# Performance work log

Hardware: AMD Instinct MI355X
Metric: run time of the kernel (lower is better)

The kernel has to match this reference:

```python
import jax, jax.numpy as jnp
import numpy as np

B, S, C, H, FF = 2, 1500, 1024, 16, 4096
D = C // H  # head_dim = 64
EPS = 1e-5


def _ln(x, g, b):
    # LayerNorm over channel dim (axis=1) for (B, C, S) tensors
    mu = jnp.mean(x, axis=1, keepdims=True)
    var = jnp.mean(jnp.square(x - mu), axis=1, keepdims=True)
    return (x - mu) * jax.lax.rsqrt(var + EPS) * g[None, :, None] + b[None, :, None]


def setup_inputs() -> dict:
    key = jax.random.key(0)
    ks = jax.random.split(key, 24)
    w = lambda k, shp: (jax.random.normal(k, shp, dtype=jnp.float32) * 0.02)
    return {
        "hidden_states": jax.random.normal(ks[0], (B, C, 1, S), dtype=jnp.float32),
        "attention_mask": jnp.ones((B, S), dtype=jnp.float32),
        "position_bias": jax.random.normal(ks[1], (B, H, S, S), dtype=jnp.float32),
        "Wq": w(ks[2], (C, C)), "bq": jnp.zeros((C,), jnp.float32),
        "Wk": w(ks[3], (C, C)), "bk": jnp.zeros((C,), jnp.float32),
        "Wv": w(ks[4], (C, C)), "bv": jnp.zeros((C,), jnp.float32),
        "Wo": w(ks[5], (C, C)), "bo": jnp.zeros((C,), jnp.float32),
        "Wg": w(ks[6], (8, D)), "bg": jnp.zeros((8,), jnp.float32),
        "gru_const": jnp.ones((1, 1, H, 1), jnp.float32),
        "ln1_g": jnp.ones((C,), jnp.float32), "ln1_b": jnp.zeros((C,), jnp.float32),
        "W1": w(ks[7], (FF, C)), "b1": jnp.zeros((FF,), jnp.float32),
        "W2": w(ks[8], (C, FF)), "b2": jnp.zeros((C,), jnp.float32),
        "ln2_g": jnp.ones((C,), jnp.float32), "ln2_b": jnp.zeros((C,), jnp.float32),
    }


def reference(hidden_states, attention_mask, position_bias,
              Wq, bq, Wk, bk, Wv, bv, Wo, bo, Wg, bg, gru_const,
              ln1_g, ln1_b, W1, b1, W2, b2, ln2_g, ln2_b):
    x = hidden_states[:, :, 0, :]  # (B, C, S)

    # --- GRU-style relative-position gate ---
    xh = x.reshape(B, H, D, S)  # (B, H, D, S)
    # conv2d with (8, D, 1, 1) kernel on (B, D, H, S) == per-head linear D->8
    g8 = jnp.einsum('od,bhds->bohs', Wg, xh) + bg[None, :, None, None]  # (B, 8, H, S)
    gate_a = jax.nn.sigmoid(jnp.sum(g8[:, :4], axis=1, keepdims=True))  # (B, 1, H, S)
    gate_b = jax.nn.sigmoid(jnp.sum(g8[:, 4:], axis=1, keepdims=True))  # (B, 1, H, S)
    gate = gate_a * (gate_b * gru_const - 1.0) + 2.0  # (B, 1, H, S)
    qk_mask = gate[:, 0, :, :, None] * position_bias  # (B, H, Sq, Sk)

    # --- self-attention ---
    q = (jnp.einsum('oc,bcs->bos', Wq, x) + bq[None, :, None]).reshape(B, H, D, S)
    k = (jnp.einsum('oc,bcs->bos', Wk, x) + bk[None, :, None]).reshape(B, H, D, S)
    v = (jnp.einsum('oc,bcs->bos', Wv, x) + bv[None, :, None]).reshape(B, H, D, S)
    scale = 1.0 / jnp.sqrt(jnp.float32(D))
    kpm = (1.0 - attention_mask) * -10000.0  # (B, S)
    scores = jnp.einsum('bhdq,bhdk->bhqk', q, k) * scale + qk_mask + kpm[:, None, None, :]
    probs = jax.nn.softmax(scores, axis=-1)
    ctx = jnp.einsum('bhqk,bhdk->bhdq', probs, v).reshape(B, C, S)
    attn_out = jnp.einsum('oc,bcs->bos', Wo, ctx) + bo[None, :, None]

    h = _ln(x + attn_out, ln1_g, ln1_b)

    # --- FFN ---
    f = jax.nn.gelu(jnp.einsum('fc,bcs->bfs', W1, h) + b1[None, :, None], approximate=False)
    f = jnp.einsum('cf,bfs->bcs', W2, f) + b2[None, :, None]

    out = _ln(h + f, ln2_g, ln2_b)
    return out[:, :, None, :]  # (B, C, 1, S)
```

## Files before the change

kernel.cpp:

```cpp
#include <hip/hip_runtime.h>
#include <cstddef>
#include <cstdint>

#define Bn 2
#define Sn 1500
#define SPn 1536
#define Cn 1024
#define Hn 16
#define FFn 4096

typedef __attribute__((ext_vector_type(8))) short bf16x8;
typedef __attribute__((ext_vector_type(4))) float f32x4;
typedef unsigned short u16;
typedef unsigned int u32;

__device__ __forceinline__ u16 f2bu(float f) {
  unsigned u = __float_as_uint(f);
  return (u16)((u + 0x7fffu + ((u >> 16) & 1u)) >> 16);
}
__device__ __forceinline__ float bu2f(u16 v) {
  return __uint_as_float(((u32)v) << 16);
}

__device__ __forceinline__ void gl_lds16(const u16* g, u16* l) {
  __builtin_amdgcn_global_load_lds(
      (__attribute__((address_space(1))) void*)(uintptr_t)g,
      (__attribute__((address_space(3))) void*)(u32)(uintptr_t)l,
      16, 0, 0);
}

__global__ __launch_bounds__(256) void k_pre(
    const float* __restrict__ x,
    const float* __restrict__ Wq, const float* __restrict__ Wk,
    const float* __restrict__ Wv, const float* __restrict__ Wo,
    const float* __restrict__ W1, const float* __restrict__ W2,
    const float* __restrict__ bq, const float* __restrict__ bk,
    const float* __restrict__ bv,
    const float* __restrict__ Wg, const float* __restrict__ bg,
    const float* __restrict__ gc,
    float* __restrict__ xT, u16* __restrict__ xTb,
    u16* __restrict__ wqkvb, u16* __restrict__ wob,
    u16* __restrict__ w1b, u16* __restrict__ w2b, float* __restrict__ bqkv,
    float* __restrict__ gate)
{
  const int bid = blockIdx.x;
  if (bid < 3072) {
    __shared__ float t[32][33];
    const int c0 = (bid & 31) * 32, s0 = ((bid >> 5) % 48) * 32, b = bid / 1536;
    const int tx = threadIdx.x & 31, ty = threadIdx.x >> 5;
#pragma unroll
    for (int i = 0; i < 32; i += 8) {
      int c = c0 + ty + i, s = s0 + tx;
      t[ty + i][tx] = (s < Sn) ? x[((size_t)b * Cn + c) * Sn + s] : 0.f;
    }
    __syncthreads();
#pragma unroll
    for (int i = 0; i < 32; i += 8) {
      int s = s0 + ty + i, c = c0 + tx;
      float v = t[tx][ty + i];
      size_t o = ((size_t)b * SPn + s) * Cn + c;
      xT[o] = v;
      xTb[o] = f2bu(v);
    }
    return;
  }
  if (bid < 15363) {
    int i = (bid - 3072) * 256 + threadIdx.x;
    const float* src;
    u16* dst;
    int j;
    if (i < 786432) {
      src = (i < 262144) ? Wq : ((i < 524288) ? Wk : Wv);
      j = i & 262143;
      dst = wqkvb + (size_t)i * 4;
    } else if (i < 1048576) {
      src = Wo; j = i - 786432; dst = wob + (size_t)j * 4;
    } else if (i < 2097152) {
      src = W1; j = i - 1048576; dst = w1b + (size_t)j * 4;
    } else if (i < 3145728) {
      src = W2; j = i - 2097152; dst = w2b + (size_t)j * 4;
    } else {
      int k = i - 3145728;
      const float* bsrc = (k < 256) ? bq : ((k < 512) ? bk : bv);
      float4 v = *(const float4*)(bsrc + (k & 255) * 4);
      *(float4*)(bqkv + k * 4) = v;
      return;
    }
    float4 v = *(const float4*)(src + (size_t)j * 4);
    ushort4 o;
    o.x = f2bu(v.x); o.y = f2bu(v.y); o.z = f2bu(v.z); o.w = f2bu(v.w);
    *(ushort4*)dst = o;
    return;
  }
  {
    const int gid = bid - 15363;
    const int b = gid / 96, h = (gid / 6) & 15;
    const int s = (gid % 6) * 256 + threadIdx.x;
    const bool vld = s < Sn;
    const float* xp = x + ((size_t)b * Cn + h * 64) * Sn + (vld ? s : 0);
    float dot[8];
#pragma unroll
    for (int o = 0; o < 8; o++) dot[o] = 0.f;
    for (int d = 0; d < 64; d++) {
      float v = xp[(size_t)d * Sn];
#pragma unroll
      for (int o = 0; o < 8; o++) dot[o] += Wg[o * 64 + d] * v;
    }
    float sa = dot[0] + dot[1] + dot[2] + dot[3] + bg[0] + bg[1] + bg[2] + bg[3];
    float sb = dot[4] + dot[5] + dot[6] + dot[7] + bg[4] + bg[5] + bg[6] + bg[7];
    float ga = 1.f / (1.f + __expf(-sa));
    float gb = 1.f / (1.f + __expf(-sb));
    float gv = ga * (gb * gc[h] - 1.f) + 2.f;
    gate[((size_t)b * Hn + h) * SPn + s] = vld ? gv : 0.f;
  }
}

__global__ __launch_bounds__(256) void k_transpose_out(
    const float* __restrict__ oT, float* __restrict__ o)
{
  __shared__ float t[32][33];
  const int b = blockIdx.z, c0 = blockIdx.x * 32, s0 = blockIdx.y * 32;
  const int tx = threadIdx.x & 31, ty = threadIdx.x >> 5;
#pragma unroll
  for (int i = 0; i < 32; i += 8) {
    int s = s0 + ty + i, c = c0 + tx;
    t[ty + i][tx] = oT[((size_t)b * SPn + s) * Cn + c];
  }
  __syncthreads();
#pragma unroll
  for (int i = 0; i < 32; i += 8) {
    int c = c0 + ty + i, s = s0 + tx;
    if (s < Sn) o[((size_t)b * Cn + c) * Sn + s] = t[tx][ty + i];
  }
}

template <int EPI, int SPLIT, int TM>
__global__ __launch_bounds__(256) void k_gemm(
    const u16* __restrict__ A, const u16* __restrict__ X,
    const float* __restrict__ bias, void* __restrict__ out, void* __restrict__ out2,
    u16* __restrict__ vT, int M, int Kst, int Ktot)
{
  constexpr int NI = TM / 32;
  const int zz = blockIdx.z;
  const int b = zz / SPLIT, half = zz % SPLIT;
  const int Kc = Ktot / SPLIT;
  const int m0 = blockIdx.x * TM;
  const int s0 = blockIdx.y * 128;
  const int tid = threadIdx.x;
  const int lane = tid & 63;
  const int wid = tid >> 6;
  const int wm = (wid >> 1) * (TM / 2);
  const int wn = (wid & 1) * 64;
  const int l15 = lane & 15;
  const int g4 = lane >> 4;

  __shared__ __align__(16) u16 lA[TM][64];
  __shared__ __align__(16) u16 lX[128][64];

  f32x4 acc[NI][4];
  f32x4 zr; zr[0] = 0.f; zr[1] = 0.f; zr[2] = 0.f; zr[3] = 0.f;
#pragma unroll
  for (int i = 0; i < NI; i++)
#pragma unroll
    for (int j = 0; j < 4; j++) acc[i][j] = zr;

  const int rlo = lane >> 3;
  const int cg = (lane & 7) ^ rlo;
  const int kbeg = half * Kc;
  const u16* gA = A + (size_t)(m0 + wid * (TM / 4) + rlo) * Kst + cg * 8 + kbeg;
  const u16* gX = X + ((size_t)b * SPn + s0 + wid * 32 + rlo) * Kst + cg * 8 + kbeg;
  u16* lAp = &lA[0][0] + wid * (TM / 4) * 64;
  u16* lXp = &lX[0][0] + wid * 2048;
  const size_t rstep8 = (size_t)8 * Kst;

  for (int kt = 0; kt < Kc; kt += 64) {
    __syncthreads();
#pragma unroll
    for (int j = 0; j < TM / 32; j++)
      gl_lds16(gA + j * rstep8 + kt, lAp + j * 512);
#pragma unroll
    for (int j = 0; j < 4; j++)
      gl_lds16(gX + j * rstep8 + kt, lXp + j * 512);
    __syncthreads();
#pragma unroll
    for (int ks = 0; ks < 2; ks++) {
      bf16x8 af[NI], bfr[4];
#pragma unroll
      for (int i = 0; i < NI; i++) {
        int ra = wm + i * 16 + l15;
        af[i] = *(const bf16x8*)&lA[ra][((ks * 4 + g4) ^ (ra & 7)) * 8];
      }
#pragma unroll
      for (int j = 0; j < 4; j++) {
        int rb = wn + j * 16 + l15;
        bfr[j] = *(const bf16x8*)&lX[rb][((ks * 4 + g4) ^ (rb & 7)) * 8];
      }
#pragma unroll
      for (int i = 0; i < NI; i++)
#pragma unroll
        for (int j = 0; j < 4; j++)
          acc[i][j] = __builtin_amdgcn_mfma_f32_16x16x32_bf16(af[i], bfr[j], acc[i][j], 0, 0, 0);
    }
  }

  const float hsc = (half == 0) ? 1.f : 0.f;
  void* outp = (half == 0) ? out : out2;
#pragma unroll
  for (int i = 0; i < NI; i++) {
    int o = m0 + wm + i * 16 + g4 * 4;
    float4 bs = *(const float4*)(bias + o);
#pragma unroll
    for (int j = 0; j < 4; j++) {
      int s = s0 + wn + j * 16 + l15;
      size_t oidx = ((size_t)b * SPn + s) * M + o;
      f32x4 v = acc[i][j];
      float x0 = v[0] + bs.x * hsc, x1 = v[1] + bs.y * hsc;
      float x2 = v[2] + bs.z * hsc, x3 = v[3] + bs.w * hsc;
      if (EPI == 0) {
        float4 st; st.x = x0; st.y = x1; st.z = x2; st.w = x3;
        *(float4*)((float*)outp + oidx) = st;
      } else if (EPI == 1) {
        x0 = 0.5f * x0 * (1.f + erff(x0 * 0.70710678118654752f));
        x1 = 0.5f * x1 * (1.f + erff(x1 * 0.70710678118654752f));
        x2 = 0.5f * x2 * (1.f + erff(x2 * 0.70710678118654752f));
        x3 = 0.5f * x3 * (1.f + erff(x3 * 0.70710678118654752f));
        ushort4 st;
        st.x = f2bu(x0); st.y = f2bu(x1); st.z = f2bu(x2); st.w = f2bu(x3);
        *(ushort4*)((u16*)outp + oidx) = st;
      } else {
        ushort4 st;
        st.x = f2bu(x0); st.y = f2bu(x1); st.z = f2bu(x2); st.w = f2bu(x3);
        *(ushort4*)((u16*)outp + oidx) = st;
        if (vT != nullptr && o >= 2048) {
          int oo = o - 2048;
          int h = oo >> 6, d = oo & 63;
          u16* vp = vT + ((size_t)(b * Hn + h) * 64 + d) * SPn + s;
          vp[0] = st.x;
          vp[SPn] = st.y;
          vp[2 * SPn] = st.z;
          vp[3 * SPn] = st.w;
        }
      }
    }
  }
}

__global__ __launch_bounds__(256) void k_flash_mfma(
    const u16* __restrict__ qkv,
    const u16* __restrict__ vT,
    const float* __restrict__ pb,
    const float* __restrict__ am,
    const float* __restrict__ gate,
    u16* __restrict__ ctx)
{
  const int bh = blockIdx.y, b = bh >> 4, h = bh & 15;
  const int q0 = blockIdx.x * 64;
  const int tid = threadIdx.x;
  const int lane = tid & 63, wid = tid >> 6;
  const int l15 = lane & 15, g4 = lane >> 4;
  const int q = q0 + wid * 16 + l15;

  __shared__ __align__(16) u16 kls[64][72];
  __shared__ __align__(16) u16 vls[64][72];
  __shared__ __align__(16) u16 pls[4][16][72];
  __shared__ float kpm[SPn];

  const int r0 = tid >> 3, c80 = (tid & 7) * 8;
  const int r1 = (256 + tid) >> 3, c81 = c80;
  const u16* kg0 = qkv + ((size_t)b * SPn + r0) * 3072 + 1024 + h * 64 + c80;
  const u16* kg1 = qkv + ((size_t)b * SPn + r1) * 3072 + 1024 + h * 64 + c81;
  const u16* vg0 = vT + ((size_t)bh * 64 + r0) * SPn + c80;
  const u16* vg1 = vT + ((size_t)bh * 64 + r1) * SPn + c81;

  bf16x8 qf[2];
  {
    const u16* qp = qkv + ((size_t)b * SPn + q) * 3072 + h * 64 + g4 * 8;
    qf[0] = *(const bf16x8*)qp;
    qf[1] = *(const bf16x8*)(qp + 32);
  }
  const float gr = gate[(size_t)bh * SPn + q];
  const int qpb = (q < Sn) ? q : (Sn - 1);
  const float* pbrow = pb + ((size_t)bh * Sn + qpb) * Sn;

  {
    int4 k0v = *(const int4*)kg0;
    int4 k1v = *(const int4*)kg1;
    int4 v0v = *(const int4*)vg0;
    int4 v1v = *(const int4*)vg1;
#pragma unroll
    for (int j = 0; j < 6; j++) {
      int idx = tid + j * 256;
      kpm[idx] = (idx < Sn) ? (1.f - am[b * Sn + idx]) * -10000.f : -1e30f;
    }
    *(int4*)&kls[r0][c80] = k0v;
    *(int4*)&kls[r1][c81] = k1v;
    *(int4*)&vls[r0][c80] = v0v;
    *(int4*)&vls[r1][c81] = v1v;
  }
  __syncthreads();

  float m = -3.0e38f, l = 0.f;
  f32x4 accO[4];
  f32x4 zr; zr[0] = 0.f; zr[1] = 0.f; zr[2] = 0.f; zr[3] = 0.f;
#pragma unroll
  for (int i = 0; i < 4; i++) accO[i] = zr;

  for (int kt = 0; kt < 24; kt++) {
    const int k0 = kt * 64;
    int4 krn0, krn1, vrn0, vrn1;
    if (kt < 23) {
      const int k0n = k0 + 64;
      krn0 = *(const int4*)(kg0 + (size_t)k0n * 3072);
      krn1 = *(const int4*)(kg1 + (size_t)k0n * 3072);
      vrn0 = *(const int4*)(vg0 + k0n);
      vrn1 = *(const int4*)(vg1 + k0n);
    }
    float4 pbv[4];
    if (kt < 23) {
#pragma unroll
      for (int km = 0; km < 4; km++)
        pbv[km] = *(const float4*)(pbrow + k0 + km * 16 + g4 * 4);
    } else {
#pragma unroll
      for (int km = 0; km < 4; km++) {
        int kk = k0 + km * 16 + g4 * 4;
        pbv[km].x = (kk + 0 < Sn) ? pbrow[kk + 0] : 0.f;
        pbv[km].y = (kk + 1 < Sn) ? pbrow[kk + 1] : 0.f;
        pbv[km].z = (kk + 2 < Sn) ? pbrow[kk + 2] : 0.f;
        pbv[km].w = (kk + 3 < Sn) ? pbrow[kk + 3] : 0.f;
      }
    }

    f32x4 sAcc[4];
#pragma unroll
    for (int km = 0; km < 4; km++) {
      sAcc[km] = zr;
#pragma unroll
      for (int dc = 0; dc < 2; dc++) {
        bf16x8 af = *(const bf16x8*)&kls[km * 16 + l15][dc * 32 + g4 * 8];
        sAcc[km] = __builtin_amdgcn_mfma_f32_16x16x32_bf16(af, qf[dc], sAcc[km], 0, 0, 0);
      }
    }

    float sc[16];
#pragma unroll
    for (int km = 0; km < 4; km++) {
      int kk = k0 + km * 16 + g4 * 4;
      float4 kp = *(const float4*)&kpm[kk];
      sc[km * 4 + 0] = sAcc[km][0] * 0.125f + gr * pbv[km].x + kp.x;
      sc[km * 4 + 1] = sAcc[km][1] * 0.125f + gr * pbv[km].y + kp.y;
      sc[km * 4 + 2] = sAcc[km][2] * 0.125f + gr * pbv[km].z + kp.z;
      sc[km * 4 + 3] = sAcc[km][3] * 0.125f + gr * pbv[km].w + kp.w;
    }

    float mloc = sc[0];
#pragma unroll
    for (int i = 1; i < 16; i++) mloc = fmaxf(mloc, sc[i]);
    mloc = fmaxf(mloc, __shfl_xor(mloc, 16));
    mloc = fmaxf(mloc, __shfl_xor(mloc, 32));

    if (mloc > m + 8.f) {
      float corr = __expf(m - mloc);
      m = mloc;
      l *= corr;
#pragma unroll
      for (int i = 0; i < 4; i++) {
        accO[i][0] *= corr; accO[i][1] *= corr;
        accO[i][2] *= corr; accO[i][3] *= corr;
      }
    }

    float ls = 0.f;
#pragma unroll
    for (int i = 0; i < 16; i++) {
      float p = __expf(sc[i] - m);
      sc[i] = p;
      ls += p;
    }
    ls += __shfl_xor(ls, 16);
    ls += __shfl_xor(ls, 32);
    l += ls;

#pragma unroll
    for (int km = 0; km < 4; km++) {
      u32 lo = (u32)f2bu(sc[km * 4 + 0]) | ((u32)f2bu(sc[km * 4 + 1]) << 16);
      u32 hi = (u32)f2bu(sc[km * 4 + 2]) | ((u32)f2bu(sc[km * 4 + 3]) << 16);
      u32* dst = (u32*)&pls[wid][l15][km * 16 + g4 * 4];
      dst[0] = lo; dst[1] = hi;
    }

    bf16x8 pf[2];
    pf[0] = *(const bf16x8*)&pls[wid][l15][g4 * 8];
    pf[1] = *(const bf16x8*)&pls[wid][l15][32 + g4 * 8];
#pragma unroll
    for (int dm = 0; dm < 4; dm++) {
#pragma unroll
      for (int kc = 0; kc < 2; kc++) {
        bf16x8 af = *(const bf16x8*)&vls[dm * 16 + l15][kc * 32 + g4 * 8];
        accO[dm] = __builtin_amdgcn_mfma_f32_16x16x32_bf16(af, pf[kc], accO[dm], 0, 0, 0);
      }
    }

    __syncthreads();
    if (kt < 23) {
      *(int4*)&kls[r0][c80] = krn0;
      *(int4*)&kls[r1][c81] = krn1;
      *(int4*)&vls[r0][c80] = vrn0;
      *(int4*)&vls[r1][c81] = vrn1;
      __syncthreads();
    }
  }

  float inv = 1.f / l;
  const bool qv = q < Sn;
#pragma unroll
  for (int dm = 0; dm < 4; dm++) {
    ushort4 st;
    st.x = f2bu(qv ? accO[dm][0] * inv : 0.f);
    st.y = f2bu(qv ? accO[dm][1] * inv : 0.f);
    st.z = f2bu(qv ? accO[dm][2] * inv : 0.f);
    st.w = f2bu(qv ? accO[dm][3] * inv : 0.f);
    *(ushort4*)(ctx + ((size_t)b * SPn + q) * Cn + h * 64 + dm * 16 + g4 * 4) = st;
  }
}

__global__ __launch_bounds__(256) void k_ln3(
    const float* __restrict__ r1, const u16* __restrict__ r2,
    const u16* __restrict__ r3,
    const float* __restrict__ g, const float* __restrict__ be,
    float* __restrict__ outF, u16* __restrict__ outB)
{
  const int s = blockIdx.x, b = blockIdx.y;
  const size_t base = ((size_t)b * SPn + s) * Cn;
  __shared__ float red[8];
  const int tid = threadIdx.x;
  const int c = tid * 4;
  float4 a = *(const float4*)(r1 + base + c);
  ushort4 v2 = *(const ushort4*)(r2 + base + c);
  ushort4 v3 = *(const ushort4*)(r3 + base + c);
  float t0 = a.x + bu2f(v2.x) + bu2f(v3.x);
  float t1 = a.y + bu2f(v2.y) + bu2f(v3.y);
  float t2 = a.z + bu2f(v2.z) + bu2f(v3.z);
  float t3 = a.w + bu2f(v2.w) + bu2f(v3.w);
  float sum = t0 + t1 + t2 + t3;
#pragma unroll
  for (int mk = 1; mk < 64; mk <<= 1) sum += __shfl_xor(sum, mk);
  if ((tid & 63) == 0) red[tid >> 6] = sum;
  __syncthreads();
  float mu = (red[0] + red[1] + red[2] + red[3]) * (1.f / Cn);
  float d0 = t0 - mu, d1 = t1 - mu, d2 = t2 - mu, d3 = t3 - mu;
  float vs = d0 * d0 + d1 * d1 + d2 * d2 + d3 * d3;
#pragma unroll
  for (int mk = 1; mk < 64; mk <<= 1) vs += __shfl_xor(vs, mk);
  if ((tid & 63) == 0) red[4 + (tid >> 6)] = vs;
  __syncthreads();
  float var = (red[4] + red[5] + red[6] + red[7]) * (1.f / Cn);
  float rstd = rsqrtf(var + 1e-5f);
  float4 gv = *(const float4*)(g + c);
  float4 bv = *(const float4*)(be + c);
  float o0 = d0 * rstd * gv.x + bv.x;
  float o1 = d1 * rstd * gv.y + bv.y;
  float o2 = d2 * rstd * gv.z + bv.z;
  float o3 = d3 * rstd * gv.w + bv.w;
  float4 st; st.x = o0; st.y = o1; st.z = o2; st.w = o3;
  *(float4*)(outF + base + c) = st;
  if (outB) {
    ushort4 sb;
    sb.x = f2bu(o0); sb.y = f2bu(o1); sb.z = f2bu(o2); sb.w = f2bu(o3);
    *(ushort4*)(outB + base + c) = sb;
  }
}

extern "C" void kernel_launch(void* const* d_in, const int* in_sizes, int n_in,
                              void* d_out, int out_size, void* d_ws, size_t ws_size,
                              hipStream_t stream)
{
  const float* x    = (const float*)d_in[0];
  const float* am   = (const float*)d_in[1];
  const float* pb   = (const float*)d_in[2];
  const float* Wq   = (const float*)d_in[3];
  const float* bq   = (const float*)d_in[4];
  const float* Wk   = (const float*)d_in[5];
  const float* bk   = (const float*)d_in[6];
  const float* Wv   = (const float*)d_in[7];
  const float* bv   = (const float*)d_in[8];
  const float* Wo   = (const float*)d_in[9];
  const float* bo   = (const float*)d_in[10];
  const float* Wg   = (const float*)d_in[11];
  const float* bg   = (const float*)d_in[12];
  const float* gc   = (const float*)d_in[13];
  const float* ln1g = (const float*)d_in[14];
  const float* ln1b = (const float*)d_in[15];
  const float* W1   = (const float*)d_in[16];
  const float* b1   = (const float*)d_in[17];
  const float* W2   = (const float*)d_in[18];
  const float* b2   = (const float*)d_in[19];
  const float* ln2g = (const float*)d_in[20];
  const float* ln2b = (const float*)d_in[21];

  char* ws = (char*)d_ws;
  float* xT     = (float*)(ws + 0);
  u16*   xTb    = (u16*)(ws + 12582912);
  u16*   wqkvb  = (u16*)(ws + 18874368);
  u16*   wob    = (u16*)(ws + 25165824);
  u16*   w1b    = (u16*)(ws + 27262976);
  u16*   w2b    = (u16*)(ws + 35651584);
  float* bqkv   = (float*)(ws + 44040192);
  float* gate   = (float*)(ws + 44052480);
  u16*   qkvB   = (u16*)(ws + 44249088);
  u16*   vT     = (u16*)(ws + 63123456);
  u16*   attnTa = (u16*)(ws + 69414912);
  u16*   attnTb = (u16*)(ws + 81997824);
  u16*   ctxT   = xTb;
  float* hT     = (float*)(ws + 44249088);
  u16*   hTb    = wqkvb;
  u16*   fT     = (u16*)(ws + 56832000);
  u16*   f2Ta   = (u16*)(ws + 0);
  u16*   f2Tb   = (u16*)(ws + 81997824);
  float* outT   = (float*)(ws + 12582912);

  dim3 blk(256);
  k_pre<<<dim3(15555), blk, 0, stream>>>(x, Wq, Wk, Wv, Wo, W1, W2, bq, bk, bv,
                                         Wg, bg, gc, xT, xTb, wqkvb, wob, w1b,
                                         w2b, bqkv, gate);

  k_gemm<2, 1, 96><<<dim3(32, 12, Bn), blk, 0, stream>>>(
      wqkvb, xTb, bqkv, qkvB, qkvB, vT, 3072, 1024, 1024);
  k_flash_mfma<<<dim3(SPn / 64, Bn * Hn), blk, 0, stream>>>(qkvB, vT, pb, am, gate, ctxT);
  k_gemm<2, 2, 64><<<dim3(16, 12, Bn * 2), blk, 0, stream>>>(
      wob, ctxT, bo, attnTa, attnTb, (u16*)nullptr, 1024, 1024, 1024);
  k_ln3<<<dim3(SPn, Bn), blk, 0, stream>>>(xT, attnTa, attnTb, ln1g, ln1b, hT, hTb);
  k_gemm<1, 1, 128><<<dim3(32, 12, Bn), blk, 0, stream>>>(
      w1b, hTb, b1, fT, fT, (u16*)nullptr, 4096, 1024, 1024);
  k_gemm<2, 2, 64><<<dim3(16, 12, Bn * 2), blk, 0, stream>>>(
      w2b, fT, b2, f2Ta, f2Tb, (u16*)nullptr, 1024, 4096, 4096);
  k_ln3<<<dim3(SPn, Bn), blk, 0, stream>>>(hT, f2Ta, f2Tb, ln2g, ln2b, outT, (u16*)nullptr);
  k_transpose_out<<<dim3(Cn / 32, SPn / 32, Bn), blk, 0, stream>>>(outT, (float*)d_out);
}
```

Before: 267.6 us.

## Coalesce position-bias loads via LDS staging and reorder prep blocks

The flash-attention kernel now loads position_bias with each 16-lane group reading a contiguous 64-float row segment, stages it in a padded LDS tile, and reads it back in the MFMA output layout. Before, each lane read scattered float4s from its own row. The goal is better global coalescing on the largest input tensor, at the cost of extra LDS traffic and space. The change also adds s_setprio around the MFMA blocks, moves the gate computation blocks to the front of the prep kernel, and skips writing the V columns into the qkv buffer since they are only read from vT.

```diff
diff --git a/kernel.cpp b/kernel.cpp
--- a/kernel.cpp
+++ b/kernel.cpp
@@ -44,9 +44,33 @@
     float* __restrict__ gate)
 {
   const int bid = blockIdx.x;
-  if (bid < 3072) {
+  if (bid < 192) {
+    const int gid = bid;
+    const int b = gid / 96, h = (gid / 6) & 15;
+    const int s = (gid % 6) * 256 + threadIdx.x;
+    const bool vld = s < Sn;
+    const float* xp = x + ((size_t)b * Cn + h * 64) * Sn + (vld ? s : 0);
+    float dot[8];
+#pragma unroll
+    for (int o = 0; o < 8; o++) dot[o] = 0.f;
+#pragma unroll 4
+    for (int d = 0; d < 64; d++) {
+      float v = xp[(size_t)d * Sn];
+#pragma unroll
+      for (int o = 0; o < 8; o++) dot[o] += Wg[o * 64 + d] * v;
+    }
+    float sa = dot[0] + dot[1] + dot[2] + dot[3] + bg[0] + bg[1] + bg[2] + bg[3];
+    float sb = dot[4] + dot[5] + dot[6] + dot[7] + bg[4] + bg[5] + bg[6] + bg[7];
+    float ga = 1.f / (1.f + __expf(-sa));
+    float gb = 1.f / (1.f + __expf(-sb));
+    float gv = ga * (gb * gc[h] - 1.f) + 2.f;
+    gate[((size_t)b * Hn + h) * SPn + s] = vld ? gv : 0.f;
+    return;
+  }
+  if (bid < 3264) {
     __shared__ float t[32][33];
-    const int c0 = (bid & 31) * 32, s0 = ((bid >> 5) % 48) * 32, b = bid / 1536;
+    const int tb = bid - 192;
+    const int c0 = (tb & 31) * 32, s0 = ((tb >> 5) % 48) * 32, b = tb / 1536;
     const int tx = threadIdx.x & 31, ty = threadIdx.x >> 5;
 #pragma unroll
     for (int i = 0; i < 32; i += 8) {
@@ -64,8 +88,8 @@
     }
     return;
   }
-  if (bid < 15363) {
-    int i = (bid - 3072) * 256 + threadIdx.x;
+  {
+    int i = (bid - 3264) * 256 + threadIdx.x;
     const float* src;
     u16* dst;
     int j;
@@ -90,28 +114,6 @@
     ushort4 o;
     o.x = f2bu(v.x); o.y = f2bu(v.y); o.z = f2bu(v.z); o.w = f2bu(v.w);
     *(ushort4*)dst = o;
-    return;
-  }
-  {
-    const int gid = bid - 15363;
-    const int b = gid / 96, h = (gid / 6) & 15;
-    const int s = (gid % 6) * 256 + threadIdx.x;
-    const bool vld = s < Sn;
-    const float* xp = x + ((size_t)b * Cn + h * 64) * Sn + (vld ? s : 0);
-    float dot[8];
-#pragma unroll
-    for (int o = 0; o < 8; o++) dot[o] = 0.f;
-    for (int d = 0; d < 64; d++) {
-      float v = xp[(size_t)d * Sn];
-#pragma unroll
-      for (int o = 0; o < 8; o++) dot[o] += Wg[o * 64 + d] * v;
-    }
-    float sa = dot[0] + dot[1] + dot[2] + dot[3] + bg[0] + bg[1] + bg[2] + bg[3];
-    float sb = dot[4] + dot[5] + dot[6] + dot[7] + bg[4] + bg[5] + bg[6] + bg[7];
-    float ga = 1.f / (1.f + __expf(-sa));
-    float gb = 1.f / (1.f + __expf(-sb));
-    float gv = ga * (gb * gc[h] - 1.f) + 2.f;
-    gate[((size_t)b * Hn + h) * SPn + s] = vld ? gv : 0.f;
   }
 }
 
@@ -230,7 +232,6 @@
       } else {
         ushort4 st;
         st.x = f2bu(x0); st.y = f2bu(x1); st.z = f2bu(x2); st.w = f2bu(x3);
-        *(ushort4*)((u16*)outp + oidx) = st;
         if (vT != nullptr && o >= 2048) {
           int oo = o - 2048;
           int h = oo >> 6, d = oo & 63;
@@ -239,6 +240,8 @@
           vp[SPn] = st.y;
           vp[2 * SPn] = st.z;
           vp[3 * SPn] = st.w;
+        } else {
+          *(ushort4*)((u16*)outp + oidx) = st;
         }
       }
     }
@@ -263,6 +266,7 @@
   __shared__ __align__(16) u16 kls[64][72];
   __shared__ __align__(16) u16 vls[64][72];
   __shared__ __align__(16) u16 pls[4][16][72];
+  __shared__ float pbs[4][16][69];
   __shared__ float kpm[SPn];
 
   const int r0 = tid >> 3, c80 = (tid & 7) * 8;
@@ -272,6 +276,16 @@
   const u16* vg0 = vT + ((size_t)bh * 64 + r0) * SPn + c80;
   const u16* vg1 = vT + ((size_t)bh * 64 + r1) * SPn + c81;
 
+  const int prow = lane >> 4;
+  const int pcol = l15 * 4;
+  int pbq[4];
+#pragma unroll
+  for (int j = 0; j < 4; j++) {
+    int qq = q0 + wid * 16 + j * 4 + prow;
+    pbq[j] = (qq < Sn) ? qq : (Sn - 1);
+  }
+  const float* pbbase = pb + (size_t)bh * Sn * Sn;
+
   bf16x8 qf[2];
   {
     const u16* qp = qkv + ((size_t)b * SPn + q) * 3072 + h * 64 + g4 * 8;
@@ -279,8 +293,6 @@
     qf[1] = *(const bf16x8*)(qp + 32);
   }
   const float gr = gate[(size_t)bh * SPn + q];
-  const int qpb = (q < Sn) ? q : (Sn - 1);
-  const float* pbrow = pb + ((size_t)bh * Sn + qpb) * Sn;
 
   {
     int4 k0v = *(const int4*)kg0;
@@ -315,23 +327,28 @@
       vrn0 = *(const int4*)(vg0 + k0n);
       vrn1 = *(const int4*)(vg1 + k0n);
     }
-    float4 pbv[4];
     if (kt < 23) {
 #pragma unroll
-      for (int km = 0; km < 4; km++)
-        pbv[km] = *(const float4*)(pbrow + k0 + km * 16 + g4 * 4);
+      for (int j = 0; j < 4; j++) {
+        float4 pv = *(const float4*)(pbbase + (size_t)pbq[j] * Sn + k0 + pcol);
+        *(float4*)&pbs[wid][j * 4 + prow][pcol] = pv;
+      }
     } else {
 #pragma unroll
-      for (int km = 0; km < 4; km++) {
-        int kk = k0 + km * 16 + g4 * 4;
-        pbv[km].x = (kk + 0 < Sn) ? pbrow[kk + 0] : 0.f;
-        pbv[km].y = (kk + 1 < Sn) ? pbrow[kk + 1] : 0.f;
-        pbv[km].z = (kk + 2 < Sn) ? pbrow[kk + 2] : 0.f;
-        pbv[km].w = (kk + 3 < Sn) ? pbrow[kk + 3] : 0.f;
+      for (int j = 0; j < 4; j++) {
+        float4 pv;
+        int kk = k0 + pcol;
+        const float* pr = pbbase + (size_t)pbq[j] * Sn;
+        pv.x = (kk + 0 < Sn) ? pr[kk + 0] : 0.f;
+        pv.y = (kk + 1 < Sn) ? pr[kk + 1] : 0.f;
+        pv.z = (kk + 2 < Sn) ? pr[kk + 2] : 0.f;
+        pv.w = (kk + 3 < Sn) ? pr[kk + 3] : 0.f;
+        *(float4*)&pbs[wid][j * 4 + prow][pcol] = pv;
       }
     }
 
     f32x4 sAcc[4];
+    __builtin_amdgcn_s_setprio(1);
 #pragma unroll
     for (int km = 0; km < 4; km++) {
       sAcc[km] = zr;
@@ -341,16 +358,18 @@
         sAcc[km] = __builtin_amdgcn_mfma_f32_16x16x32_bf16(af, qf[dc], sAcc[km], 0, 0, 0);
       }
     }
+    __builtin_amdgcn_s_setprio(0);
 
     float sc[16];
 #pragma unroll
     for (int km = 0; km < 4; km++) {
       int kk = k0 + km * 16 + g4 * 4;
       float4 kp = *(const float4*)&kpm[kk];
-      sc[km * 4 + 0] = sAcc[km][0] * 0.125f + gr * pbv[km].x + kp.x;
-      sc[km * 4 + 1] = sAcc[km][1] * 0.125f + gr * pbv[km].y + kp.y;
-      sc[km * 4 + 2] = sAcc[km][2] * 0.125f + gr * pbv[km].z + kp.z;
-      sc[km * 4 + 3] = sAcc[km][3] * 0.125f + gr * pbv[km].w + kp.w;
+      float4 pbv = *(const float4*)&pbs[wid][l15][km * 16 + g4 * 4];
+      sc[km * 4 + 0] = sAcc[km][0] * 0.125f + gr * pbv.x + kp.x;
+      sc[km * 4 + 1] = sAcc[km][1] * 0.125f + gr * pbv.y + kp.y;
+      sc[km * 4 + 2] = sAcc[km][2] * 0.125f + gr * pbv.z + kp.z;
+      sc[km * 4 + 3] = sAcc[km][3] * 0.125f + gr * pbv.w + kp.w;
     }
 
     float mloc = sc[0];
@@ -392,6 +411,7 @@
     bf16x8 pf[2];
     pf[0] = *(const bf16x8*)&pls[wid][l15][g4 * 8];
     pf[1] = *(const bf16x8*)&pls[wid][l15][32 + g4 * 8];
+    __builtin_amdgcn_s_setprio(1);
 #pragma unroll
     for (int dm = 0; dm < 4; dm++) {
 #pragma unroll
@@ -400,6 +420,7 @@
         accO[dm] = __builtin_amdgcn_mfma_f32_16x16x32_bf16(af, pf[kc], accO[dm], 0, 0, 0);
       }
     }
+    __builtin_amdgcn_s_setprio(0);
 
     __syncthreads();
     if (kt < 23) {
```

Measured after the change: 262.8 us. About the same (-1.8%).
